# Kernel optimization log

Measured on AMD Instinct MI355X. Metric: run time of the kernel, lower is better.

## Reference

```python
import jax, jax.numpy as jnp
from jax import lax
import numpy as np

VOCAB = 50257
EMB = 768
HID = [1024, 1024, 1024]
B, S = 2, 2048
LN_EPS_RNN = 1e-5   # torch default inside MinGRU layers
LN_EPS_OUT = 0.0    # NLPModel passes bias=False into LayerNorm's eps slot


def _layernorm(x, w, b, eps):
    mu = jnp.mean(x, axis=-1, keepdims=True)
    var = jnp.var(x, axis=-1, keepdims=True)
    return (x - mu) * lax.rsqrt(var + eps) * w + b


def _log_g(x):
    # log of g(x) = where(x>=0, x+0.5, sigmoid(x)), computed stably in log space
    return jnp.where(x >= 0, jnp.log(jax.nn.relu(x) + 0.5), -jax.nn.softplus(-x))


def _mingru_scan(gate, hidden, h0):
    # gate, hidden: [B,S,H]; h0: [B,1,H] (positive). Log-space parallel scan.
    log_coeffs = -jax.nn.softplus(gate)              # log(1-z)
    log_values = -jax.nn.softplus(-gate) + _log_g(hidden)  # log(z) + log g(h~)
    log_coeffs = jnp.pad(log_coeffs, ((0, 0), (1, 0), (0, 0)))
    log_values = jnp.concatenate([jnp.log(h0), log_values], axis=1)
    a_star = jnp.cumsum(log_coeffs, axis=1)
    log_h = a_star + lax.cumlogsumexp(log_values - a_star, axis=1)
    return jnp.exp(log_h)[:, 1:]                     # [B,S,H]


def setup_inputs() -> dict:
    key = jax.random.key(0)
    ks = jax.random.split(key, 8)
    inp = {}
    inp["ids"] = jax.random.randint(ks[0], (B, S), 0, VOCAB)
    inp["emb_W"] = jax.random.normal(ks[1], (VOCAB, EMB)) * 0.02
    dims = [EMB] + HID
    for l, (i, o) in enumerate(zip(dims[:-1], dims[1:])):
        inp[f"ln{l}_w"] = jnp.ones((i,))
        inp[f"ln{l}_b"] = jnp.zeros((i,))
        inp[f"gates{l}_W"] = jax.random.normal(jax.random.fold_in(key, 10 + l), (2 * o, i)) * (1.0 / np.sqrt(i))
    inp["res0_W"] = jax.random.normal(ks[2], (HID[0], EMB)) * (1.0 / np.sqrt(EMB))
    inp["lnf_w"] = jnp.ones((HID[-1],))
    inp["lnf_b"] = jnp.zeros((HID[-1],))
    inp["fc_W"] = jax.random.normal(ks[3], (VOCAB, HID[-1])) * 0.02
    inp["fc_b"] = jnp.zeros((VOCAB,))
    return inp


def reference(ids, emb_W, ln0_w, ln0_b, gates0_W, res0_W,
              ln1_w, ln1_b, gates1_W, ln2_w, ln2_b, gates2_W,
              lnf_w, lnf_b, fc_W, fc_b):
    x = emb_W[ids]                                   # [B,S,EMB]
    layers = [
        (ln0_w, ln0_b, gates0_W, res0_W),
        (ln1_w, ln1_b, gates1_W, None),
        (ln2_w, ln2_b, gates2_W, None),
    ]
    inp = x
    for ln_w, ln_b, gW, resW in layers:
        out_dim = gW.shape[0] // 2
        xn = _layernorm(inp, ln_w, ln_b, LN_EPS_RNN)
        gh = jnp.einsum('bsi,oi->bso', xn, gW)       # bias=False for minGRU
        gate, hidden = jnp.split(gh, 2, axis=-1)
        h0 = jnp.full((inp.shape[0], 1, out_dim), 0.5, dtype=inp.dtype)  # g(0)=0.5
        out = _mingru_scan(gate, hidden, h0)
        res = inp if resW is None else jnp.einsum('bsi,oi->bso', inp, resW)
        inp = out + res                              # residual, dropout=0
    x = _layernorm(inp, lnf_w, lnf_b, LN_EPS_OUT)
    logits = jnp.einsum('bsh,vh->bsv', x, fc_W) + fc_b
    return logits
```

## Files before the change

kernel.cpp:

```cpp
#include <hip/hip_runtime.h>
#include <stdint.h>
#include <stddef.h>


typedef __attribute__((ext_vector_type(4))) float f32x4;
typedef __attribute__((ext_vector_type(8))) short bf16x8;
typedef float f32x4u __attribute__((vector_size(16), aligned(4)));

__device__ __forceinline__ unsigned short f2bf(float f) {
  unsigned int u = __float_as_uint(f);
  u += 0x7FFFu + ((u >> 16) & 1u);
  return (unsigned short)(u >> 16);
}

__device__ __forceinline__ void gload16(const void* g, void* l) {
  __builtin_amdgcn_global_load_lds(
      (const __attribute__((address_space(1))) void*)g,
      (__attribute__((address_space(3))) void*)l, 16, 0, 0);
}

__global__ __launch_bounds__(256) void cvt_kernel(
    const float* __restrict__ in, unsigned short* __restrict__ out, int n8) {
  int i = blockIdx.x * 256 + threadIdx.x;
  int stride = gridDim.x * 256;
  for (; i < n8; i += stride) {
    const float4* p = (const float4*)in + (size_t)i * 2;
    float4 a = p[0], b = p[1];
    bf16x8 o;
    o[0] = (short)f2bf(a.x); o[1] = (short)f2bf(a.y);
    o[2] = (short)f2bf(a.z); o[3] = (short)f2bf(a.w);
    o[4] = (short)f2bf(b.x); o[5] = (short)f2bf(b.y);
    o[6] = (short)f2bf(b.z); o[7] = (short)f2bf(b.w);
    *(bf16x8*)(out + (size_t)i * 8) = o;
  }
}

__global__ __launch_bounds__(256) void embed_kernel(
    const int* __restrict__ ids, const float* __restrict__ embW,
    unsigned short* __restrict__ xbf) {
  int tok = blockIdx.x;
  int id = ids[tok];
  const float* src = embW + (size_t)id * 768;
  unsigned short* dst = xbf + (size_t)tok * 768;
  for (int j = threadIdx.x; j < 768; j += 256) dst[j] = f2bf(src[j]);
}

template <int BF16IN, int D>
__global__ __launch_bounds__(256) void ln_kernel(
    const void* __restrict__ xin, const float* __restrict__ w,
    const float* __restrict__ b, unsigned short* __restrict__ xout,
    float eps) {
  constexpr int NV = D / 256;
  int row = blockIdx.x;
  int tid = threadIdx.x;
  int lane = tid & 63, wid = tid >> 6;
  const float* xf = (const float*)xin;
  const unsigned short* xb = (const unsigned short*)xin;
  float vals[NV];
  float s = 0.f, ss = 0.f;
#pragma unroll
  for (int i = 0; i < NV; i++) {
    size_t idx = (size_t)row * D + i * 256 + tid;
    float v;
    if (BF16IN) {
      unsigned int u = ((unsigned int)xb[idx]) << 16;
      v = __uint_as_float(u);
    } else {
      v = xf[idx];
    }
    vals[i] = v;
    s += v;
    ss += v * v;
  }
  for (int off = 32; off; off >>= 1) {
    s += __shfl_down(s, off);
    ss += __shfl_down(ss, off);
  }
  __shared__ float red[8];
  if (lane == 0) { red[wid] = s; red[4 + wid] = ss; }
  __syncthreads();
  s = red[0] + red[1] + red[2] + red[3];
  ss = red[4] + red[5] + red[6] + red[7];
  constexpr float invD = 1.f / (float)D;
  float mu = s * invD;
  float var = ss * invD - mu * mu;
  float inv = rsqrtf(var + eps);
#pragma unroll
  for (int i = 0; i < NV; i++) {
    int col = i * 256 + tid;
    size_t idx = (size_t)row * D + col;
    float y = (vals[i] - mu) * inv * w[col] + b[col];
    xout[idx] = f2bf(y);
  }
}

__global__ __launch_bounds__(256) void gemm_bt(
    const unsigned short* __restrict__ A, const unsigned short* __restrict__ B,
    float* __restrict__ C, int M, int N, int K) {
  __shared__ __align__(16) char smem[16896];
  unsigned short* lsA = (unsigned short*)smem;
  unsigned short* lsB = (unsigned short*)(smem + 8192);
  float* lsC = (float*)smem;

  const int tid = threadIdx.x;
  const int lane = tid & 63;
  const int wid = __builtin_amdgcn_readfirstlane(tid >> 6);
  const int row0 = blockIdx.y * 128;
  const int col0 = blockIdx.x * 128;

  const int srow = tid >> 2;
  const int skg = (tid & 3) * 8;

  const unsigned short* gA0 = A + (size_t)(row0 + srow) * K + skg;
  const unsigned short* gA1 = A + (size_t)(row0 + 64 + srow) * K + skg;
  const unsigned short* gB0 = B + (size_t)(col0 + srow) * K + skg;
  const unsigned short* gB1 = B + (size_t)(col0 + 64 + srow) * K + skg;

  char* ldsA0 = (char*)lsA + wid * 1024;
  char* ldsA1 = (char*)lsA + 4096 + wid * 1024;
  char* ldsB0 = (char*)lsB + wid * 1024;
  char* ldsB1 = (char*)lsB + 4096 + wid * 1024;

  const int wm = wid >> 1, wn = wid & 1;
  const unsigned short* pA = lsA + (wm * 64 + (lane & 15)) * 32 + (lane >> 4) * 8;
  const unsigned short* pB = lsB + (wn * 64 + (lane & 15)) * 32 + (lane >> 4) * 8;

  f32x4 acc[4][4] = {};

  for (int k0 = 0; k0 < K; k0 += 32) {
    gload16(gA0 + k0, ldsA0);
    gload16(gA1 + k0, ldsA1);
    gload16(gB0 + k0, ldsB0);
    gload16(gB1 + k0, ldsB1);
    __syncthreads();
    bf16x8 af[4], bfr[4];
#pragma unroll
    for (int i = 0; i < 4; i++) af[i] = *(const bf16x8*)(pA + i * 512);
#pragma unroll
    for (int i = 0; i < 4; i++) bfr[i] = *(const bf16x8*)(pB + i * 512);
#pragma unroll
    for (int i = 0; i < 4; i++)
#pragma unroll
      for (int j = 0; j < 4; j++)
        acc[i][j] = __builtin_amdgcn_mfma_f32_16x16x32_bf16(bfr[j], af[i],
                                                            acc[i][j], 0, 0, 0);
    __syncthreads();
  }

  const int mloc = lane & 15;
  const int ng = (lane >> 4) * 4;
  const int LDC = 132;
  const int trow = tid >> 5;
  const int tcol = (tid & 31) * 4;
#pragma unroll
  for (int c = 0; c < 4; c++) {
    if (wm == (c >> 1)) {
      const int i0 = 2 * (c & 1);
#pragma unroll
      for (int ii = 0; ii < 2; ii++)
#pragma unroll
        for (int j = 0; j < 4; j++)
          *(f32x4*)(lsC + (ii * 16 + mloc) * LDC + wn * 64 + j * 16 + ng) =
              acc[i0 + ii][j];
    }
    __syncthreads();
#pragma unroll
    for (int rr = 0; rr < 4; rr++) {
      const int r = rr * 8 + trow;
      const size_t gr = row0 + c * 32 + r;
      f32x4 v = *(const f32x4*)(lsC + r * LDC + tcol);
      *(f32x4*)(C + gr * N + col0 + tcol) = v;
    }
    __syncthreads();
  }
}

__global__ __launch_bounds__(256) void gemm_final64(
    const unsigned short* __restrict__ A, const unsigned short* __restrict__ B,
    float* __restrict__ C, const float* __restrict__ bias, int M, int N,
    int K) {
  __shared__ __align__(16) char smem[32768];
  char* const lsA = smem;
  char* const lsB = smem + 16384;
  float* const lsC = (float*)smem;

  const int t = threadIdx.x;
  const int l = t & 63;
  const int w = __builtin_amdgcn_readfirstlane(t >> 6);
  const int row0 = blockIdx.x * 128;
  const int col0 = blockIdx.y * 128;

  const int srow = t >> 3;
  const int sg = ((t & 7) ^ (srow & 7)) * 8;
  const unsigned short* gA0 = A + (size_t)(row0 + srow) * K + sg;
  const unsigned short* gA1 = A + (size_t)(row0 + 32 + srow) * K + sg;
  const unsigned short* gA2 = A + (size_t)(row0 + 64 + srow) * K + sg;
  const unsigned short* gA3 = A + (size_t)(row0 + 96 + srow) * K + sg;
  int b0 = min(col0 + srow, N - 1);
  int b1 = min(col0 + 32 + srow, N - 1);
  int b2 = min(col0 + 64 + srow, N - 1);
  int b3 = min(col0 + 96 + srow, N - 1);
  const unsigned short* gB0 = B + (size_t)b0 * K + sg;
  const unsigned short* gB1 = B + (size_t)b1 * K + sg;
  const unsigned short* gB2 = B + (size_t)b2 * K + sg;
  const unsigned short* gB3 = B + (size_t)b3 * K + sg;
  const int wOff = w * 1024;

  const int wm = w >> 1, wn = w & 1;
  const int aRowB = (wm * 64 + (l & 15)) * 128;
  const int bRowB = (wn * 64 + (l & 15)) * 128;
  const int gk0 = (((l >> 4)) ^ (l & 7)) * 16;
  const int gk1 = ((4 + (l >> 4)) ^ (l & 7)) * 16;

  f32x4 acc[4][4] = {};

  for (int k0 = 0; k0 < K; k0 += 64) {
    gload16(gA0 + k0, lsA + wOff);
    gload16(gA1 + k0, lsA + 4096 + wOff);
    gload16(gA2 + k0, lsA + 8192 + wOff);
    gload16(gA3 + k0, lsA + 12288 + wOff);
    gload16(gB0 + k0, lsB + wOff);
    gload16(gB1 + k0, lsB + 4096 + wOff);
    gload16(gB2 + k0, lsB + 8192 + wOff);
    gload16(gB3 + k0, lsB + 12288 + wOff);
    __syncthreads();
    bf16x8 af[4][2], bfr[4][2];
#pragma unroll
    for (int i = 0; i < 4; i++) {
      af[i][0] = *(const bf16x8*)(lsA + aRowB + i * 2048 + gk0);
      af[i][1] = *(const bf16x8*)(lsA + aRowB + i * 2048 + gk1);
    }
#pragma unroll
    for (int j = 0; j < 4; j++) {
      bfr[j][0] = *(const bf16x8*)(lsB + bRowB + j * 2048 + gk0);
      bfr[j][1] = *(const bf16x8*)(lsB + bRowB + j * 2048 + gk1);
    }
#pragma unroll
    for (int i = 0; i < 4; i++)
#pragma unroll
      for (int j = 0; j < 4; j++) {
        acc[i][j] = __builtin_amdgcn_mfma_f32_16x16x32_bf16(
            bfr[j][0], af[i][0], acc[i][j], 0, 0, 0);
        acc[i][j] = __builtin_amdgcn_mfma_f32_16x16x32_bf16(
            bfr[j][1], af[i][1], acc[i][j], 0, 0, 0);
      }
    __syncthreads();
  }

  const int mloc = l & 15;
  const int ng = (l >> 4) * 4;
  const int LDC = 132;
  const int trow = t >> 5;
  const int tcol = (t & 31) * 4;
#pragma unroll
  for (int c = 0; c < 4; c++) {
    if (wm == (c >> 1)) {
      const int i0 = 2 * (c & 1);
#pragma unroll
      for (int ii = 0; ii < 2; ii++)
#pragma unroll
        for (int j = 0; j < 4; j++)
          *(f32x4*)(lsC + (ii * 16 + mloc) * LDC + wn * 64 + j * 16 + ng) =
              acc[i0 + ii][j];
    }
    __syncthreads();
#pragma unroll
    for (int rr = 0; rr < 4; rr++) {
      const int r = rr * 8 + trow;
      const size_t gr = row0 + c * 32 + r;
      f32x4 v = *(const f32x4*)(lsC + r * LDC + tcol);
      const int n0 = col0 + tcol;
      if (col0 + 128 <= N) {
        const f32x4u bv = *(const f32x4u*)(bias + n0);
        f32x4u o;
#pragma unroll
        for (int q = 0; q < 4; q++) o[q] = v[q] + bv[q];
        __builtin_nontemporal_store(o, (f32x4u*)(C + gr * N + n0));
      } else {
#pragma unroll
        for (int q = 0; q < 4; q++)
          if (n0 + q < N) C[gr * N + n0 + q] = v[q] + bias[n0 + q];
      }
    }
    __syncthreads();
  }
}

__device__ __forceinline__ void gru_step(float gate, float hid, float& a,
                                         float& g) {
  a = 1.f / (1.f + expf(gate));
  g = (hid >= 0.f) ? (hid + 0.5f) : 1.f / (1.f + expf(-hid));
}

__global__ __launch_bounds__(256) void scan_compose(
    const float* __restrict__ gh, float* __restrict__ Acl,
    float* __restrict__ Vcl) {
  int ck = blockIdx.x;
  int hp = blockIdx.y * 256 + threadIdx.x;
  int b = hp >> 10, h = hp & 1023;
  const float* gb = gh + ((size_t)(b * 2048 + ck * 64)) * 2048 + h;
  float A = 1.f, V = 0.f;
  for (int t = 0; t < 64; t++) {
    float gate = gb[(size_t)t * 2048];
    float hid = gb[(size_t)t * 2048 + 1024];
    float a, g;
    gru_step(gate, hid, a, g);
    V = a * V + (1.f - a) * g;
    A *= a;
  }
  size_t i = (size_t)(b * 32 + ck) * 1024 + h;
  Acl[i] = A;
  Vcl[i] = V;
}

__global__ __launch_bounds__(256) void scan_prefix(
    const float* __restrict__ Acl, const float* __restrict__ Vcl,
    float* __restrict__ Hin) {
  int hp = blockIdx.x * 256 + threadIdx.x;
  int b = hp >> 10, h = hp & 1023;
  float hr = 0.5f;
  for (int ck = 0; ck < 32; ck++) {
    size_t i = (size_t)(b * 32 + ck) * 1024 + h;
    Hin[i] = hr;
    hr = Acl[i] * hr + Vcl[i];
  }
}

__global__ __launch_bounds__(256) void scan_emit(
    const float* __restrict__ gh, const float* __restrict__ Hin,
    const float* __restrict__ res, float* __restrict__ xout) {
  int ck = blockIdx.x;
  int hp = blockIdx.y * 256 + threadIdx.x;
  int b = hp >> 10, h = hp & 1023;
  const float* gb = gh + ((size_t)(b * 2048 + ck * 64)) * 2048 + h;
  const float* rb = res + ((size_t)(b * 2048 + ck * 64)) * 1024 + h;
  float* ob = xout + ((size_t)(b * 2048 + ck * 64)) * 1024 + h;
  float hc = Hin[(size_t)(b * 32 + ck) * 1024 + h];
  for (int t = 0; t < 64; t++) {
    float gate = gb[(size_t)t * 2048];
    float hid = gb[(size_t)t * 2048 + 1024];
    float a, g;
    gru_step(gate, hid, a, g);
    hc = a * hc + (1.f - a) * g;
    ob[(size_t)t * 1024] = hc + rb[(size_t)t * 1024];
  }
}

extern "C" void kernel_launch(void* const* d_in, const int* in_sizes, int n_in,
                              void* d_out, int out_size, void* d_ws,
                              size_t ws_size, hipStream_t stream) {
  (void)in_sizes; (void)n_in; (void)out_size; (void)ws_size;
  const int* ids = (const int*)d_in[0];
  const float* embW = (const float*)d_in[1];
  const float* ln0w = (const float*)d_in[2];
  const float* ln0b = (const float*)d_in[3];
  const float* g0W = (const float*)d_in[4];
  const float* ln1w = (const float*)d_in[5];
  const float* ln1b = (const float*)d_in[6];
  const float* g1W = (const float*)d_in[7];
  const float* ln2w = (const float*)d_in[8];
  const float* ln2b = (const float*)d_in[9];
  const float* g2W = (const float*)d_in[10];
  const float* r0W = (const float*)d_in[11];
  const float* lnfw = (const float*)d_in[12];
  const float* lnfb = (const float*)d_in[13];
  const float* fcW = (const float*)d_in[14];
  const float* fcb = (const float*)d_in[15];
  float* out = (float*)d_out;

  const int M = 4096;
  const int V = 50257;

  char* ws = (char*)d_ws;
  unsigned short* x_bf = (unsigned short*)(ws + 0);
  float* x_f = (float*)(ws + 6291456);
  unsigned short* xn_bf = (unsigned short*)(ws + 23068672);
  float* gh = (float*)(ws + 31457280);
  float* r0 = (float*)(ws + 65011712);
  float* Acl = (float*)(ws + 81788928);
  float* Vcl = (float*)(ws + 82051072);
  float* Hin = (float*)(ws + 82313216);
  unsigned short* gwbf = (unsigned short*)(ws + 82575360);
  unsigned short* rwbf = (unsigned short*)(ws + 86769664);
  unsigned short* fcwbf = (unsigned short*)(ws + 88342528);

  auto cvt = [&](const float* src, unsigned short* dst, int n) {
    int n8 = n / 8;
    int grid = min((n8 + 255) / 256, 2048);
    cvt_kernel<<<grid, 256, 0, stream>>>(src, dst, n8);
  };

  embed_kernel<<<M, 256, 0, stream>>>(ids, embW, x_bf);
  cvt(fcW, fcwbf, V * 1024);
  cvt(r0W, rwbf, 1024 * 768);

  cvt(g0W, gwbf, 2048 * 768);
  ln_kernel<1, 768><<<M, 256, 0, stream>>>(x_bf, ln0w, ln0b, xn_bf, 1e-5f);
  gemm_bt<<<dim3(16, 32), 256, 0, stream>>>(xn_bf, gwbf, gh, M, 2048, 768);
  gemm_bt<<<dim3(8, 32), 256, 0, stream>>>(x_bf, rwbf, r0, M, 1024, 768);
  scan_compose<<<dim3(32, 8), 256, 0, stream>>>(gh, Acl, Vcl);
  scan_prefix<<<8, 256, 0, stream>>>(Acl, Vcl, Hin);
  scan_emit<<<dim3(32, 8), 256, 0, stream>>>(gh, Hin, r0, x_f);

  cvt(g1W, gwbf, 2048 * 1024);
  ln_kernel<0, 1024><<<M, 256, 0, stream>>>(x_f, ln1w, ln1b, xn_bf, 1e-5f);
  gemm_bt<<<dim3(16, 32), 256, 0, stream>>>(xn_bf, gwbf, gh, M, 2048, 1024);
  scan_compose<<<dim3(32, 8), 256, 0, stream>>>(gh, Acl, Vcl);
  scan_prefix<<<8, 256, 0, stream>>>(Acl, Vcl, Hin);
  scan_emit<<<dim3(32, 8), 256, 0, stream>>>(gh, Hin, x_f, x_f);

  cvt(g2W, gwbf, 2048 * 1024);
  ln_kernel<0, 1024><<<M, 256, 0, stream>>>(x_f, ln2w, ln2b, xn_bf, 1e-5f);
  gemm_bt<<<dim3(16, 32), 256, 0, stream>>>(xn_bf, gwbf, gh, M, 2048, 1024);
  scan_compose<<<dim3(32, 8), 256, 0, stream>>>(gh, Acl, Vcl);
  scan_prefix<<<8, 256, 0, stream>>>(Acl, Vcl, Hin);
  scan_emit<<<dim3(32, 8), 256, 0, stream>>>(gh, Hin, x_f, x_f);

  ln_kernel<0, 1024><<<M, 256, 0, stream>>>(x_f, lnfw, lnfb, xn_bf, 0.0f);
  gemm_final64<<<dim3(32, (V + 127) / 128), 256, 0, stream>>>(
      xn_bf, fcwbf, out, fcb, M, V, 1024);
}
```

Baseline: 925.8 us.

## Double-buffer LDS tiles in final vocab GEMM to overlap loads with MFMA

Gives the final logits GEMM two 32KB LDS buffers and issues the next K-tile's direct-to-LDS global loads before computing on the current tile. A partial vmcnt wait stands in for the full __syncthreads at the top of each iteration, so global memory latency can overlap with the MFMA work. LDS use per block doubles to 64KB, which may lower occupancy. The manual waitcnt and barrier ordering must be exact to stay correct.

```diff
diff --git a/kernel.cpp b/kernel.cpp
--- a/kernel.cpp
+++ b/kernel.cpp
@@ -18,6 +18,8 @@
       (const __attribute__((address_space(1))) void*)g,
       (__attribute__((address_space(3))) void*)l, 16, 0, 0);
 }
+
+#define MEMFENCE asm volatile("" ::: "memory")
 
 __global__ __launch_bounds__(256) void cvt_kernel(
     const float* __restrict__ in, unsigned short* __restrict__ out, int n8) {
@@ -179,9 +181,7 @@
     const unsigned short* __restrict__ A, const unsigned short* __restrict__ B,
     float* __restrict__ C, const float* __restrict__ bias, int M, int N,
     int K) {
-  __shared__ __align__(16) char smem[32768];
-  char* const lsA = smem;
-  char* const lsB = smem + 16384;
+  __shared__ __align__(16) char smem[65536];
   float* const lsC = (float*)smem;
 
   const int t = threadIdx.x;
@@ -214,26 +214,47 @@
 
   f32x4 acc[4][4] = {};
 
-  for (int k0 = 0; k0 < K; k0 += 64) {
-    gload16(gA0 + k0, lsA + wOff);
-    gload16(gA1 + k0, lsA + 4096 + wOff);
-    gload16(gA2 + k0, lsA + 8192 + wOff);
-    gload16(gA3 + k0, lsA + 12288 + wOff);
-    gload16(gB0 + k0, lsB + wOff);
-    gload16(gB1 + k0, lsB + 4096 + wOff);
-    gload16(gB2 + k0, lsB + 8192 + wOff);
-    gload16(gB3 + k0, lsB + 12288 + wOff);
-    __syncthreads();
+#define STAGE(BUF, KOFF)                            \
+  do {                                              \
+    char* a_ = smem + (BUF) * 32768;                \
+    char* b_ = a_ + 16384;                          \
+    gload16(gA0 + (KOFF), a_ + wOff);               \
+    gload16(gA1 + (KOFF), a_ + 4096 + wOff);        \
+    gload16(gA2 + (KOFF), a_ + 8192 + wOff);        \
+    gload16(gA3 + (KOFF), a_ + 12288 + wOff);       \
+    gload16(gB0 + (KOFF), b_ + wOff);               \
+    gload16(gB1 + (KOFF), b_ + 4096 + wOff);        \
+    gload16(gB2 + (KOFF), b_ + 8192 + wOff);        \
+    gload16(gB3 + (KOFF), b_ + 12288 + wOff);       \
+  } while (0)
+
+  STAGE(0, 0);
+
+  const int NK = K >> 6;
+  for (int kt = 0; kt < NK; ++kt) {
+    const int cur = kt & 1;
+    const char* aB = smem + cur * 32768;
+    const char* bB = aB + 16384;
+
+    if (kt + 1 < NK) {
+      STAGE(cur ^ 1, (kt + 1) << 6);
+      asm volatile("s_waitcnt vmcnt(8)" ::: "memory");
+    } else {
+      asm volatile("s_waitcnt vmcnt(0)" ::: "memory");
+    }
+    __builtin_amdgcn_s_barrier();
+    MEMFENCE;
+
     bf16x8 af[4][2], bfr[4][2];
 #pragma unroll
     for (int i = 0; i < 4; i++) {
-      af[i][0] = *(const bf16x8*)(lsA + aRowB + i * 2048 + gk0);
-      af[i][1] = *(const bf16x8*)(lsA + aRowB + i * 2048 + gk1);
+      af[i][0] = *(const bf16x8*)(aB + aRowB + i * 2048 + gk0);
+      af[i][1] = *(const bf16x8*)(aB + aRowB + i * 2048 + gk1);
     }
 #pragma unroll
     for (int j = 0; j < 4; j++) {
-      bfr[j][0] = *(const bf16x8*)(lsB + bRowB + j * 2048 + gk0);
-      bfr[j][1] = *(const bf16x8*)(lsB + bRowB + j * 2048 + gk1);
+      bfr[j][0] = *(const bf16x8*)(bB + bRowB + j * 2048 + gk0);
+      bfr[j][1] = *(const bf16x8*)(bB + bRowB + j * 2048 + gk1);
     }
 #pragma unroll
     for (int i = 0; i < 4; i++)
@@ -244,8 +265,12 @@
         acc[i][j] = __builtin_amdgcn_mfma_f32_16x16x32_bf16(
             bfr[j][1], af[i][1], acc[i][j], 0, 0, 0);
       }
-    __syncthreads();
-  }
+
+    MEMFENCE;
+    __builtin_amdgcn_s_barrier();
+    MEMFENCE;
+  }
+#undef STAGE
 
   const int mloc = l & 15;
   const int ng = (l >> 4) * 4;
```

Result: faster. 900.9 us (-2.7%).
